# Kernel tuning notes

Hardware: AMD Instinct MI355X
Metric: run time of the kernel (lower is better)

Reference implementation:

```python
import jax, jax.numpy as jnp
import numpy as np

H = 16  # num_heads
ROPE_BASE = 10000.0

def _rotate_half(x):
    d = x.shape[-1]
    return jnp.concatenate((-x[..., d // 2:], x[..., :d // 2]), axis=-1)

def setup_inputs() -> dict:
    key = jax.random.key(0)
    ks = jax.random.split(key, 9)
    B, S, E = 4, 2048, 1024
    s = 0.02
    return {
        "x": jax.random.normal(ks[0], (B, S, E), dtype=jnp.float32),
        "wq": jax.random.normal(ks[1], (E, E), dtype=jnp.float32) * s,
        "bq": jax.random.normal(ks[2], (E,), dtype=jnp.float32) * s,
        "wk": jax.random.normal(ks[3], (E, E), dtype=jnp.float32) * s,
        "bk": jax.random.normal(ks[4], (E,), dtype=jnp.float32) * s,
        "wv": jax.random.normal(ks[5], (E, E), dtype=jnp.float32) * s,
        "bv": jax.random.normal(ks[6], (E,), dtype=jnp.float32) * s,
        "wo": jax.random.normal(ks[7], (E, E), dtype=jnp.float32) * s,
        "bo": jax.random.normal(ks[8], (E,), dtype=jnp.float32) * s,
    }

def reference(x, wq, bq, wk, bk, wv, bv, wo, bo):
    B, S, E = x.shape
    D = E // H  # head_dim
    # projections (nn.Linear: x @ W.T + b), then split heads -> (B, H, S, D)
    def proj(w, b):
        return (x @ w.T + b).reshape(B, S, H, D).transpose(0, 2, 1, 3)
    q = proj(wq, bq)
    k = proj(wk, bk)
    v = proj(wv, bv)
    # RoPE: freqs (S, D//2) -> repeat_interleave(2) -> (S, D)
    inv_freq = 1.0 / (ROPE_BASE ** (jnp.arange(0, D, 2, dtype=jnp.float32) / D))
    freqs = jnp.arange(S, dtype=jnp.float32)[:, None] * inv_freq[None, :]
    cos = jnp.repeat(jnp.cos(freqs), 2, axis=-1)[None, None]  # (1,1,S,D)
    sin = jnp.repeat(jnp.sin(freqs), 2, axis=-1)[None, None]
    q = q * cos + _rotate_half(q) * sin
    k = k * cos + _rotate_half(k) * sin
    scale = D ** (-0.5)
    scores = jnp.einsum('bhqd,bhkd->bhqk', q, k) * scale
    attn = jax.nn.softmax(scores, axis=-1)
    out = jnp.einsum('bhqk,bhkd->bhqd', attn, v)  # (B,H,S,D)
    out = out.transpose(0, 2, 1, 3).reshape(B, S, E)
    return out @ wo.T + bo
```

## Files before the change

kernel.cpp:

```cpp
#include <hip/hip_runtime.h>


typedef __attribute__((ext_vector_type(4))) float f32x4;
typedef __attribute__((ext_vector_type(16))) float f32x16;
typedef __attribute__((ext_vector_type(8))) short bfrag;
typedef __attribute__((ext_vector_type(4))) short svec4;
typedef __attribute__((ext_vector_type(4))) unsigned u32x4;

#define MFMA16(a, b, c) __builtin_amdgcn_mfma_f32_16x16x32_bf16(a, b, c, 0, 0, 0)
#define MFMA32(a, b, c) __builtin_amdgcn_mfma_f32_32x32x16_bf16(a, b, c, 0, 0, 0)

__device__ __forceinline__ unsigned short f2bf(float f) {
  unsigned u = __builtin_bit_cast(unsigned, f);
  u += 0x7FFFu + ((u >> 16) & 1u);
  return (unsigned short)(u >> 16);
}

__device__ __forceinline__ void gload16(const void* g, void* l) {
  __builtin_amdgcn_global_load_lds(
      (const __attribute__((address_space(1))) unsigned int*)g,
      (__attribute__((address_space(3))) unsigned int*)l, 16, 0, 0);
}

__global__ __launch_bounds__(256) void prep_kernel(
    const float* __restrict__ x, const float* __restrict__ wq,
    const float* __restrict__ wk, const float* __restrict__ wv,
    const float* __restrict__ wo,
    unsigned short* __restrict__ xb, unsigned short* __restrict__ wqb,
    unsigned short* __restrict__ wkb, unsigned short* __restrict__ wvb,
    unsigned short* __restrict__ wob, float2* __restrict__ rope) {
  const int y = blockIdx.y;
  const int tid = blockIdx.x * blockDim.x + threadIdx.x;
  const int stride = gridDim.x * blockDim.x;
  if (y < 5) {
    const float* src = y == 0 ? x : y == 1 ? wq : y == 2 ? wk : y == 3 ? wv : wo;
    unsigned short* dst = y == 0 ? xb : y == 1 ? wqb : y == 2 ? wkb : y == 3 ? wvb : wob;
    const int n4 = (y == 0 ? (8192 * 1024) : (1024 * 1024)) >> 2;
    for (int i = tid; i < n4; i += stride) {
      float4 v = ((const float4*)src)[i];
      svec4 o;
      o.x = (short)f2bf(v.x); o.y = (short)f2bf(v.y);
      o.z = (short)f2bf(v.z); o.w = (short)f2bf(v.w);
      ((svec4*)dst)[i] = o;
    }
  } else {
    for (int i = tid; i < 2048 * 32; i += stride) {
      int s = i >> 5, f = i & 31;
      float invf = powf(10000.0f, -(float)f * (1.0f / 32.0f));
      float ang = (float)s * invf;
      rope[i] = make_float2(cosf(ang), sinf(ang));
    }
  }
}

__global__ __launch_bounds__(256) void gemm_qkv(
    const unsigned short* __restrict__ Xb,
    const unsigned short* __restrict__ Wq, const unsigned short* __restrict__ Wk,
    const unsigned short* __restrict__ Wv,
    const float* __restrict__ biasq, const float* __restrict__ biask,
    const float* __restrict__ biasv,
    const float2* __restrict__ rope,
    unsigned short* __restrict__ Qo, unsigned short* __restrict__ Ko,
    unsigned short* __restrict__ Vto) {
  const int z = blockIdx.z;
  __shared__ unsigned short As[128 * 64];
  __shared__ unsigned short Bs[128 * 64];
  const int t = threadIdx.x;
  const int lane = t & 63, w = t >> 6;
  const int wr = w >> 1, wc = w & 1;
  const int lc = lane & 15, lr = lane >> 4;

  int m0, n0;
  const unsigned short *Apt, *Bpt;
  if (z == 0)      { m0 = blockIdx.y * 128; n0 = blockIdx.x * 128; Apt = Xb; Bpt = Wq; }
  else if (z == 1) { m0 = blockIdx.y * 128; n0 = blockIdx.x * 128; Apt = Xb; Bpt = Wk; }
  else             { m0 = blockIdx.x * 128; n0 = blockIdx.y * 128; Apt = Wv; Bpt = Xb; }

  const int arow = t >> 3;
  const int acol = ((t & 7) << 3) ^ ((arow & 7) << 3);
  const unsigned short* gA = Apt + (size_t)(m0 + arow) * 1024 + acol;
  const unsigned short* gB = Bpt + (size_t)(n0 + arow) * 1024 + acol;
  unsigned short* lA = As + t * 8;
  unsigned short* lB = Bs + t * 8;

  f32x4 acc[4][4];
#pragma unroll
  for (int m = 0; m < 4; ++m)
#pragma unroll
    for (int n = 0; n < 4; ++n) acc[m][n] = (f32x4){0.f, 0.f, 0.f, 0.f};

  const int rsw = (lc & 7) << 3;

#pragma unroll 1
  for (int kt = 0; kt < 16; ++kt) {
    __syncthreads();
#pragma unroll
    for (int c = 0; c < 4; ++c) {
      gload16(gA + (size_t)c * 32 * 1024, lA + c * 2048);
      gload16(gB + (size_t)c * 32 * 1024, lB + c * 2048);
    }
    gA += 64; gB += 64;
    __syncthreads();
#pragma unroll
    for (int ks = 0; ks < 2; ++ks) {
      bfrag af[4], bfr[4];
#pragma unroll
      for (int i = 0; i < 4; ++i)
        af[i] = *(const bfrag*)(As + (wr * 64 + i * 16 + lc) * 64 + ((ks * 32 + lr * 8) ^ rsw));
#pragma unroll
      for (int i = 0; i < 4; ++i)
        bfr[i] = *(const bfrag*)(Bs + (wc * 64 + i * 16 + lc) * 64 + ((ks * 32 + lr * 8) ^ rsw));
#pragma unroll
      for (int m = 0; m < 4; ++m)
#pragma unroll
        for (int n = 0; n < 4; ++n)
          acc[m][n] = MFMA16(af[m], bfr[n], acc[m][n]);
    }
  }

  if (z < 2) {
    const float* bias = (z == 0) ? biasq : biask;
    unsigned short* dst = (z == 0) ? Qo : Ko;
    const float qs = (z == 0) ? 0.125f * 1.44269504f : 1.0f;
    const int h = (n0 + wc * 64) >> 6;
#pragma unroll
    for (int m = 0; m < 4; ++m) {
#pragma unroll
      for (int r = 0; r < 4; ++r) {
        int row = m0 + wr * 64 + m * 16 + lr * 4 + r;
        int b = row >> 11, s = row & 2047;
        const float2* trow = rope + (s << 5);
        size_t base = ((size_t)((b << 4) + h) * 2048 + s) * 64;
#pragma unroll
        for (int n = 0; n < 2; ++n) {
          int col1 = n0 + wc * 64 + n * 16 + lc;
          int d = n * 16 + lc;
          float a  = acc[m][n][r]     + bias[col1];
          float bb = acc[m][n + 2][r] + bias[col1 + 32];
          float2 t0 = trow[d >> 1];
          float2 t1 = trow[16 + (d >> 1)];
          dst[base + d]      = f2bf((a * t0.x - bb * t0.y) * qs);
          dst[base + d + 32] = f2bf((bb * t1.x + a * t1.y) * qs);
        }
      }
    }
  } else {
#pragma unroll
    for (int m = 0; m < 4; ++m) {
#pragma unroll
      for (int r = 0; r < 4; ++r) {
        int wcol = m0 + wr * 64 + m * 16 + lr * 4 + r;
        float bv = biasv[wcol];
        int h = wcol >> 6, d = wcol & 63;
#pragma unroll
        for (int n = 0; n < 4; ++n) {
          int token = n0 + wc * 64 + n * 16 + lc;
          int b = token >> 11, s = token & 2047;
          Vto[((size_t)((b << 4) + h) * 64 + d) * 2048 + s] = f2bf(acc[m][n][r] + bv);
        }
      }
    }
  }
}

__global__ __launch_bounds__(256) void attn_kernel(
    const unsigned short* __restrict__ Q, const unsigned short* __restrict__ K,
    const unsigned short* __restrict__ Vt, unsigned short* __restrict__ O) {
  __shared__ unsigned short Ks[2][64 * 64];
  __shared__ unsigned short Vs[2][64 * 64];
  const int t = threadIdx.x;
  const int lane = t & 63, w = t >> 6;
  const int l31 = lane & 31, th = lane >> 5;
  const int bid = blockIdx.x;
  const int xcd = bid & 7;
  const int jj = bid >> 3;
  const int bh = xcd * 8 + (jj >> 4);
  const int qb = jj & 15;
  const int q0 = qb * 128 + w * 32;

  const unsigned short* Qp = Q + ((size_t)bh * 2048 + q0 + l31) * 64 + th * 8;
  bfrag bq[4];
#pragma unroll
  for (int kk = 0; kk < 4; ++kk) bq[kk] = *(const bfrag*)(Qp + kk * 16);

  f32x16 accO0, accO1;
#pragma unroll
  for (int i = 0; i < 16; ++i) { accO0[i] = 0.f; accO1[i] = 0.f; }
  float lsum = 0.f;

  const unsigned short* Kg = K + (size_t)bh * 2048 * 64;
  const unsigned short* Vg = Vt + (size_t)bh * 64 * 2048;

  const int rs = (l31 & 7) << 3;

  const int srow = t >> 3;
  const int scol = ((t & 7) ^ (srow & 7)) << 3;

#define STAGE(bufi, kb_)                                                        \
  {                                                                             \
    gload16(Kg + (size_t)((kb_) + srow) * 64 + scol,        Ks[bufi] + t * 8);  \
    gload16(Kg + (size_t)((kb_) + 32 + srow) * 64 + scol,   Ks[bufi] + 2048 + t * 8); \
    gload16(Vg + (size_t)srow * 2048 + (kb_) + scol,        Vs[bufi] + t * 8);  \
    gload16(Vg + (size_t)(32 + srow) * 2048 + (kb_) + scol, Vs[bufi] + 2048 + t * 8); \
  }

  STAGE(0, 0);
  STAGE(1, 64);
  int cur = 0;

#pragma unroll 1
  for (int kt = 0; kt < 32; ++kt) {
    if (kt < 30) { asm volatile("s_waitcnt vmcnt(4)" ::: "memory"); }
    else         { asm volatile("s_waitcnt vmcnt(0)" ::: "memory"); }
    __builtin_amdgcn_s_barrier();

    const unsigned short* KsC = Ks[cur];
    const unsigned short* VsC = Vs[cur];

    bfrag pa[4];

#pragma unroll
    for (int kb = 0; kb < 2; ++kb) {
      f32x16 sc;
#pragma unroll
      for (int i = 0; i < 16; ++i) sc[i] = 0.f;
      const unsigned short* kp = KsC + (kb * 32 + l31) * 64;
      __builtin_amdgcn_s_setprio(1);
#pragma unroll
      for (int kk = 0; kk < 4; ++kk) {
        bfrag ka = *(const bfrag*)(kp + ((kk * 16 + th * 8) ^ rs));
        sc = MFMA32(ka, bq[kk], sc);
      }
      __builtin_amdgcn_s_setprio(0);

#pragma unroll
      for (int i = 0; i < 16; ++i) sc[i] = __builtin_amdgcn_exp2f(sc[i]);
      {
        float s0 = (sc[0] + sc[1]) + (sc[2] + sc[3]);
        float s1 = (sc[4] + sc[5]) + (sc[6] + sc[7]);
        float s2 = (sc[8] + sc[9]) + (sc[10] + sc[11]);
        float s3 = (sc[12] + sc[13]) + (sc[14] + sc[15]);
        lsum += (s0 + s1) + (s2 + s3);
      }

      unsigned pk[4][2];
#pragma unroll
      for (int g = 0; g < 4; ++g) {
        asm("v_cvt_pk_bf16_f32 %0, %1, %2"
            : "=v"(pk[g][0]) : "v"(sc[4 * g]), "v"(sc[4 * g + 1]));
        asm("v_cvt_pk_bf16_f32 %0, %1, %2"
            : "=v"(pk[g][1]) : "v"(sc[4 * g + 2]), "v"(sc[4 * g + 3]));
      }

#pragma unroll
      for (int ka = 0; ka < 2; ++ka) {
        u32x4 pu;
#pragma unroll
        for (int j = 0; j < 2; ++j) {
          unsigned zlo = pk[2 * ka][j];
          unsigned zhi = pk[2 * ka + 1][j];
          unsigned zsend = th ? zlo : zhi;
          unsigned wv = (unsigned)__shfl_xor((int)zsend, 32);
          pu[j]     = th ? wv : zlo;
          pu[2 + j] = th ? zhi : wv;
        }
        pa[kb * 2 + ka] = __builtin_bit_cast(bfrag, pu);
      }
    }

    __builtin_amdgcn_s_setprio(1);
#pragma unroll
    for (int kg = 0; kg < 4; ++kg) {
      const unsigned short* vp0 = VsC + (size_t)l31 * 64;
      const unsigned short* vp1 = VsC + (size_t)(32 + l31) * 64;
      bfrag vb0 = *(const bfrag*)(vp0 + ((kg * 16 + th * 8) ^ rs));
      bfrag vb1 = *(const bfrag*)(vp1 + ((kg * 16 + th * 8) ^ rs));
      accO0 = MFMA32(pa[kg], vb0, accO0);
      accO1 = MFMA32(pa[kg], vb1, accO1);
    }
    __builtin_amdgcn_s_setprio(0);

    __builtin_amdgcn_s_barrier();
    if (kt + 2 < 32) STAGE(cur, (kt + 2) * 64);
    cur ^= 1;
  }
#undef STAGE

  float v = lsum + __shfl_xor(lsum, 32);
  float inv = 1.0f / v;

  const int b = bh >> 4, h = bh & 15;
#pragma unroll
  for (int r = 0; r < 16; ++r) {
    int qrow = (r & 3) + 8 * (r >> 2) + 4 * th;
    float invr = __shfl(inv, qrow);
    size_t base = (((size_t)b * 2048 + q0 + qrow) * 16 + h) * 64 + l31;
    O[base]      = f2bf(accO0[r] * invr);
    O[base + 32] = f2bf(accO1[r] * invr);
  }
}

__global__ __launch_bounds__(256) void gemm_out(
    const unsigned short* __restrict__ Ob, const unsigned short* __restrict__ Wo,
    const float* __restrict__ bias, float* __restrict__ out) {
  __shared__ unsigned short As[128 * 64];
  __shared__ unsigned short Bs[128 * 64];
  const int t = threadIdx.x;
  const int lane = t & 63, w = t >> 6;
  const int wr = w >> 1, wc = w & 1;
  const int lc = lane & 15, lr = lane >> 4;
  const int m0 = blockIdx.y * 128, n0 = blockIdx.x * 128;

  const int arow = t >> 3;
  const int acol = ((t & 7) << 3) ^ ((arow & 7) << 3);
  const unsigned short* gA = Ob + (size_t)(m0 + arow) * 1024 + acol;
  const unsigned short* gB = Wo + (size_t)(n0 + arow) * 1024 + acol;
  unsigned short* lA = As + t * 8;
  unsigned short* lB = Bs + t * 8;

  f32x4 acc[4][4];
#pragma unroll
  for (int m = 0; m < 4; ++m)
#pragma unroll
    for (int n = 0; n < 4; ++n) acc[m][n] = (f32x4){0.f, 0.f, 0.f, 0.f};

  const int rsw = (lc & 7) << 3;

#pragma unroll 1
  for (int kt = 0; kt < 16; ++kt) {
    __syncthreads();
#pragma unroll
    for (int c = 0; c < 4; ++c) {
      gload16(gA + (size_t)c * 32 * 1024, lA + c * 2048);
      gload16(gB + (size_t)c * 32 * 1024, lB + c * 2048);
    }
    gA += 64; gB += 64;
    __syncthreads();
#pragma unroll
    for (int ks = 0; ks < 2; ++ks) {
      bfrag af[4], bfr[4];
#pragma unroll
      for (int i = 0; i < 4; ++i)
        af[i] = *(const bfrag*)(As + (wr * 64 + i * 16 + lc) * 64 + ((ks * 32 + lr * 8) ^ rsw));
#pragma unroll
      for (int i = 0; i < 4; ++i)
        bfr[i] = *(const bfrag*)(Bs + (wc * 64 + i * 16 + lc) * 64 + ((ks * 32 + lr * 8) ^ rsw));
#pragma unroll
      for (int m = 0; m < 4; ++m)
#pragma unroll
        for (int n = 0; n < 4; ++n)
          acc[m][n] = MFMA16(af[m], bfr[n], acc[m][n]);
    }
  }
#pragma unroll
  for (int n = 0; n < 4; ++n) {
    int col = n0 + wc * 64 + n * 16 + lc;
    float bv = bias[col];
#pragma unroll
    for (int m = 0; m < 4; ++m) {
#pragma unroll
      for (int r = 0; r < 4; ++r) {
        int row = m0 + wr * 64 + m * 16 + lr * 4 + r;
        out[(size_t)row * 1024 + col] = acc[m][n][r] + bv;
      }
    }
  }
}

extern "C" void kernel_launch(void* const* d_in, const int* in_sizes, int n_in,
                              void* d_out, int out_size, void* d_ws, size_t ws_size,
                              hipStream_t stream) {
  (void)in_sizes; (void)n_in; (void)out_size; (void)ws_size;
  const float* x  = (const float*)d_in[0];
  const float* wq = (const float*)d_in[1];
  const float* bq = (const float*)d_in[2];
  const float* wk = (const float*)d_in[3];
  const float* bk = (const float*)d_in[4];
  const float* wv = (const float*)d_in[5];
  const float* bv = (const float*)d_in[6];
  const float* wo = (const float*)d_in[7];
  const float* bo = (const float*)d_in[8];
  float* out = (float*)d_out;

  char* ws = (char*)d_ws;
  unsigned short* Xb   = (unsigned short*)(ws);
  unsigned short* Wqb  = (unsigned short*)(ws + (16ull << 20));
  unsigned short* Wkb  = (unsigned short*)(ws + (18ull << 20));
  unsigned short* Wvb  = (unsigned short*)(ws + (20ull << 20));
  unsigned short* Wob  = (unsigned short*)(ws + (22ull << 20));
  unsigned short* Qb   = (unsigned short*)(ws + (24ull << 20));
  unsigned short* Kb   = (unsigned short*)(ws + (40ull << 20));
  unsigned short* Vt   = (unsigned short*)(ws + (56ull << 20));
  float2* rope         = (float2*)(ws + (72ull << 20));
  unsigned short* Ob   = Xb;

  prep_kernel<<<dim3(1024, 6), 256, 0, stream>>>(x, wq, wk, wv, wo,
                                                 Xb, Wqb, Wkb, Wvb, Wob, rope);
  gemm_qkv<<<dim3(8, 64, 3), 256, 0, stream>>>(Xb, Wqb, Wkb, Wvb,
                                               bq, bk, bv, rope, Qb, Kb, Vt);
  attn_kernel<<<1024, 256, 0, stream>>>(Qb, Kb, Vt, Ob);
  gemm_out<<<dim3(8, 64), 256, 0, stream>>>(Ob, Wob, bo, out);
}
```

Before: 221.6 us.

## Process two 32-row query tiles per wave in attention kernel

Each wave now handles 64 query rows as two 32-row sub-tiles, so every block covers 256 queries and the grid is halved to 512 blocks. K and V fragments read from LDS are reused across both sub-tiles, and the K/V global loads per query are halved. The cost is roughly double the accumulator and score registers per lane, which may lower occupancy. It also leaves fewer blocks to spread across the compute units.

New measurement: 206.1 us. 1.08x faster.

```diff
diff --git a/kernel.cpp b/kernel.cpp
--- a/kernel.cpp
+++ b/kernel.cpp
@@ -174,19 +174,24 @@
   const int bid = blockIdx.x;
   const int xcd = bid & 7;
   const int jj = bid >> 3;
-  const int bh = xcd * 8 + (jj >> 4);
-  const int qb = jj & 15;
-  const int q0 = qb * 128 + w * 32;
+  const int bh = xcd * 8 + (jj >> 3);
+  const int qb = jj & 7;
+  const int q0 = qb * 256 + w * 64;
 
   const unsigned short* Qp = Q + ((size_t)bh * 2048 + q0 + l31) * 64 + th * 8;
-  bfrag bq[4];
-#pragma unroll
-  for (int kk = 0; kk < 4; ++kk) bq[kk] = *(const bfrag*)(Qp + kk * 16);
-
-  f32x16 accO0, accO1;
-#pragma unroll
-  for (int i = 0; i < 16; ++i) { accO0[i] = 0.f; accO1[i] = 0.f; }
-  float lsum = 0.f;
+  bfrag bq0[4], bq1[4];
+#pragma unroll
+  for (int kk = 0; kk < 4; ++kk) {
+    bq0[kk] = *(const bfrag*)(Qp + kk * 16);
+    bq1[kk] = *(const bfrag*)(Qp + 32 * 64 + kk * 16);
+  }
+
+  f32x16 acc00, acc01, acc10, acc11;
+#pragma unroll
+  for (int i = 0; i < 16; ++i) {
+    acc00[i] = 0.f; acc01[i] = 0.f; acc10[i] = 0.f; acc11[i] = 0.f;
+  }
+  float lsum0 = 0.f, lsum1 = 0.f;
 
   const unsigned short* Kg = K + (size_t)bh * 2048 * 64;
   const unsigned short* Vg = Vt + (size_t)bh * 64 * 2048;
@@ -217,54 +222,61 @@
     const unsigned short* KsC = Ks[cur];
     const unsigned short* VsC = Vs[cur];
 
-    bfrag pa[4];
+    bfrag pa0[4], pa1[4];
 
 #pragma unroll
     for (int kb = 0; kb < 2; ++kb) {
-      f32x16 sc;
-#pragma unroll
-      for (int i = 0; i < 16; ++i) sc[i] = 0.f;
       const unsigned short* kp = KsC + (kb * 32 + l31) * 64;
-      __builtin_amdgcn_s_setprio(1);
-#pragma unroll
-      for (int kk = 0; kk < 4; ++kk) {
-        bfrag ka = *(const bfrag*)(kp + ((kk * 16 + th * 8) ^ rs));
-        sc = MFMA32(ka, bq[kk], sc);
-      }
-      __builtin_amdgcn_s_setprio(0);
-
-#pragma unroll
-      for (int i = 0; i < 16; ++i) sc[i] = __builtin_amdgcn_exp2f(sc[i]);
-      {
-        float s0 = (sc[0] + sc[1]) + (sc[2] + sc[3]);
-        float s1 = (sc[4] + sc[5]) + (sc[6] + sc[7]);
-        float s2 = (sc[8] + sc[9]) + (sc[10] + sc[11]);
-        float s3 = (sc[12] + sc[13]) + (sc[14] + sc[15]);
-        lsum += (s0 + s1) + (s2 + s3);
-      }
-
-      unsigned pk[4][2];
-#pragma unroll
-      for (int g = 0; g < 4; ++g) {
-        asm("v_cvt_pk_bf16_f32 %0, %1, %2"
-            : "=v"(pk[g][0]) : "v"(sc[4 * g]), "v"(sc[4 * g + 1]));
-        asm("v_cvt_pk_bf16_f32 %0, %1, %2"
-            : "=v"(pk[g][1]) : "v"(sc[4 * g + 2]), "v"(sc[4 * g + 3]));
-      }
-
-#pragma unroll
-      for (int ka = 0; ka < 2; ++ka) {
-        u32x4 pu;
-#pragma unroll
-        for (int j = 0; j < 2; ++j) {
-          unsigned zlo = pk[2 * ka][j];
-          unsigned zhi = pk[2 * ka + 1][j];
-          unsigned zsend = th ? zlo : zhi;
-          unsigned wv = (unsigned)__shfl_xor((int)zsend, 32);
-          pu[j]     = th ? wv : zlo;
-          pu[2 + j] = th ? zhi : wv;
+      bfrag ka[4];
+#pragma unroll
+      for (int kk = 0; kk < 4; ++kk)
+        ka[kk] = *(const bfrag*)(kp + ((kk * 16 + th * 8) ^ rs));
+
+#pragma unroll
+      for (int g = 0; g < 2; ++g) {
+        f32x16 sc;
+#pragma unroll
+        for (int i = 0; i < 16; ++i) sc[i] = 0.f;
+        __builtin_amdgcn_s_setprio(1);
+#pragma unroll
+        for (int kk = 0; kk < 4; ++kk)
+          sc = MFMA32(ka[kk], g == 0 ? bq0[kk] : bq1[kk], sc);
+        __builtin_amdgcn_s_setprio(0);
+
+#pragma unroll
+        for (int i = 0; i < 16; ++i) sc[i] = __builtin_amdgcn_exp2f(sc[i]);
+        {
+          float s0 = (sc[0] + sc[1]) + (sc[2] + sc[3]);
+          float s1 = (sc[4] + sc[5]) + (sc[6] + sc[7]);
+          float s2 = (sc[8] + sc[9]) + (sc[10] + sc[11]);
+          float s3 = (sc[12] + sc[13]) + (sc[14] + sc[15]);
+          if (g == 0) lsum0 += (s0 + s1) + (s2 + s3);
+          else        lsum1 += (s0 + s1) + (s2 + s3);
         }
-        pa[kb * 2 + ka] = __builtin_bit_cast(bfrag, pu);
+
+        unsigned pk[4][2];
+#pragma unroll
+        for (int gg = 0; gg < 4; ++gg) {
+          asm("v_cvt_pk_bf16_f32 %0, %1, %2"
+              : "=v"(pk[gg][0]) : "v"(sc[4 * gg]), "v"(sc[4 * gg + 1]));
+          asm("v_cvt_pk_bf16_f32 %0, %1, %2"
+              : "=v"(pk[gg][1]) : "v"(sc[4 * gg + 2]), "v"(sc[4 * gg + 3]));
+        }
+#pragma unroll
+        for (int ka2 = 0; ka2 < 2; ++ka2) {
+          u32x4 pu;
+#pragma unroll
+          for (int j = 0; j < 2; ++j) {
+            unsigned zlo = pk[2 * ka2][j];
+            unsigned zhi = pk[2 * ka2 + 1][j];
+            unsigned zsend = th ? zlo : zhi;
+            unsigned wv = (unsigned)__shfl_xor((int)zsend, 32);
+            pu[j]     = th ? wv : zlo;
+            pu[2 + j] = th ? zhi : wv;
+          }
+          if (g == 0) pa0[kb * 2 + ka2] = __builtin_bit_cast(bfrag, pu);
+          else        pa1[kb * 2 + ka2] = __builtin_bit_cast(bfrag, pu);
+        }
       }
     }
 
@@ -275,8 +287,10 @@
       const unsigned short* vp1 = VsC + (size_t)(32 + l31) * 64;
       bfrag vb0 = *(const bfrag*)(vp0 + ((kg * 16 + th * 8) ^ rs));
       bfrag vb1 = *(const bfrag*)(vp1 + ((kg * 16 + th * 8) ^ rs));
-      accO0 = MFMA32(pa[kg], vb0, accO0);
-      accO1 = MFMA32(pa[kg], vb1, accO1);
+      acc00 = MFMA32(pa0[kg], vb0, acc00);
+      acc01 = MFMA32(pa0[kg], vb1, acc01);
+      acc10 = MFMA32(pa1[kg], vb0, acc10);
+      acc11 = MFMA32(pa1[kg], vb1, acc11);
     }
     __builtin_amdgcn_s_setprio(0);
 
@@ -286,17 +300,23 @@
   }
 #undef STAGE
 
-  float v = lsum + __shfl_xor(lsum, 32);
-  float inv = 1.0f / v;
+  float v0 = lsum0 + __shfl_xor(lsum0, 32);
+  float v1 = lsum1 + __shfl_xor(lsum1, 32);
+  float inv0 = 1.0f / v0;
+  float inv1 = 1.0f / v1;
 
   const int b = bh >> 4, h = bh & 15;
 #pragma unroll
   for (int r = 0; r < 16; ++r) {
     int qrow = (r & 3) + 8 * (r >> 2) + 4 * th;
-    float invr = __shfl(inv, qrow);
-    size_t base = (((size_t)b * 2048 + q0 + qrow) * 16 + h) * 64 + l31;
-    O[base]      = f2bf(accO0[r] * invr);
-    O[base + 32] = f2bf(accO1[r] * invr);
+    float invr0 = __shfl(inv0, qrow);
+    float invr1 = __shfl(inv1, qrow);
+    size_t base0 = (((size_t)b * 2048 + q0 + qrow) * 16 + h) * 64 + l31;
+    size_t base1 = (((size_t)b * 2048 + q0 + 32 + qrow) * 16 + h) * 64 + l31;
+    O[base0]      = f2bf(acc00[r] * invr0);
+    O[base0 + 32] = f2bf(acc01[r] * invr0);
+    O[base1]      = f2bf(acc10[r] * invr1);
+    O[base1 + 32] = f2bf(acc11[r] * invr1);
   }
 }
 
@@ -398,6 +418,6 @@
                                                  Xb, Wqb, Wkb, Wvb, Wob, rope);
   gemm_qkv<<<dim3(8, 64, 3), 256, 0, stream>>>(Xb, Wqb, Wkb, Wvb,
                                                bq, bk, bv, rope, Qb, Kb, Vt);
-  attn_kernel<<<1024, 256, 0, stream>>>(Qb, Kb, Vt, Ob);
+  attn_kernel<<<512, 256, 0, stream>>>(Qb, Kb, Vt, Ob);
   gemm_out<<<dim3(8, 64), 256, 0, stream>>>(Ob, Wob, bo, out);
 }
```
